# Optimization experiments

Measured on AMD Instinct MI355X. Metric: run time of the kernel, lower is better.

The kernel has to match this reference:

```python
import jax, jax.numpy as jnp
import numpy as np

N_NODES = 100000
N_EDGES = 3200000
IN_FEATS = 128
HIDDEN = 8
HEADS = 4
OUT_FEATS = 1
NEG_SLOPE = 0.2


def setup_inputs() -> dict:
    key = jax.random.key(0)
    ks = jax.random.split(key, 12)
    x = jax.random.normal(ks[0], (N_NODES, IN_FEATS), dtype=jnp.float32)
    edge_index = jax.random.randint(ks[1], (2, N_EDGES), 0, N_NODES, dtype=jnp.int64)
    # conv1: in=128 -> heads=4, out=8 (concat)
    s1 = 1.0 / np.sqrt(IN_FEATS)
    W1 = jax.random.uniform(ks[2], (IN_FEATS, HEADS * HIDDEN), jnp.float32, -s1, s1)
    att_src1 = jax.random.normal(ks[3], (HEADS, HIDDEN), dtype=jnp.float32) * 0.1
    att_dst1 = jax.random.normal(ks[4], (HEADS, HIDDEN), dtype=jnp.float32) * 0.1
    b1 = jnp.zeros((HEADS * HIDDEN,), jnp.float32)
    # conv2: in=32 -> heads=1, out=1 (no concat)
    s2 = 1.0 / np.sqrt(HEADS * HIDDEN)
    W2 = jax.random.uniform(ks[5], (HEADS * HIDDEN, 1 * OUT_FEATS), jnp.float32, -s2, s2)
    att_src2 = jax.random.normal(ks[6], (1, OUT_FEATS), dtype=jnp.float32) * 0.1
    att_dst2 = jax.random.normal(ks[7], (1, OUT_FEATS), dtype=jnp.float32) * 0.1
    b2 = jnp.zeros((OUT_FEATS,), jnp.float32)
    return {"x": x, "edge_index": edge_index,
            "W1": W1, "att_src1": att_src1, "att_dst1": att_dst1, "b1": b1,
            "W2": W2, "att_src2": att_src2, "att_dst2": att_dst2, "b2": b2}


def gat_conv(x, src, dst, W, a_src, a_dst, b, heads, out_ch, concat):
    """PyG GATConv (eval mode: dropout identity), self-loops already included in src/dst."""
    N = x.shape[0]
    h = (x @ W).reshape(N, heads, out_ch)                 # [N,H,C]
    alpha_s = jnp.sum(h * a_src[None], axis=-1)           # [N,H]
    alpha_d = jnp.sum(h * a_dst[None], axis=-1)           # [N,H]
    e = jax.nn.leaky_relu(alpha_s[src] + alpha_d[dst], NEG_SLOPE)  # [E,H]
    # segment softmax over incoming edges per destination node
    m = jax.ops.segment_max(e, dst, num_segments=N)       # [N,H]; every node has a self-loop
    ex = jnp.exp(e - m[dst])
    denom = jax.ops.segment_sum(ex, dst, num_segments=N)
    alpha = ex / denom[dst]                               # [E,H]
    msg = alpha[:, :, None] * h[src]                      # [E,H,C]
    agg = jax.ops.segment_sum(msg, dst, num_segments=N)   # [N,H,C]
    if concat:
        agg = agg.reshape(N, heads * out_ch)
    else:
        agg = agg.mean(axis=1)
    return agg + b


def reference(x, edge_index, W1, att_src1, att_dst1, b1, W2, att_src2, att_dst2, b2):
    N = x.shape[0]
    loops = jnp.arange(N, dtype=edge_index.dtype)
    src = jnp.concatenate([edge_index[0], loops])
    dst = jnp.concatenate([edge_index[1], loops])
    h = gat_conv(x, src, dst, W1, att_src1, att_dst1, b1, HEADS, HIDDEN, True)
    h = jax.nn.elu(h)
    out = gat_conv(h, src, dst, W2, att_src2, att_dst2, b2, 1, OUT_FEATS, False)
    return out
```

## Files before the change

kernel.cpp:

```cpp
#include <hip/hip_runtime.h>
#include <hip/hip_fp16.h>

#define NEG_SLOPE 0.2f
#define LOG2E 1.4426950408889634f
#define NC 782
#define TILE 6144
#define CAP 4736

__device__ __forceinline__ int uclamp(int i, int n) {
    return ((unsigned)i < (unsigned)n) ? i : 0;
}


__global__ __launch_bounds__(512) void k_msplit(const int* __restrict__ ei, int* __restrict__ gcur,
                                                int* __restrict__ ebin, int E, int N) {
    __shared__ int hist[NC], lpre[NC], lcur[NC];
    __shared__ int tbuf[TILE];
    __shared__ unsigned short tcb[TILE];
    __shared__ int part[512];
    int t = threadIdx.x;
    int tb = blockIdx.x * TILE;
    int nt = E - tb; if (nt > TILE) nt = TILE; if (nt < 0) nt = 0;
    for (int i = t; i < NC; i += 512) { hist[i] = 0; lcur[i] = 0; }
    __syncthreads();
    int sv[12]; short cbv[12];
#pragma unroll
    for (int j = 0; j < 12; ++j) {
        int idx = tb + j * 512 + t;
        int cb = -1, v = 0;
        if (idx < E) {
            int s = uclamp(ei[idx], N), d = uclamp(ei[E + idx], N);
            cb = d >> 7;
            v = (s << 7) | (d & 127);
            atomicAdd(&hist[cb], 1);
        }
        sv[j] = v; cbv[j] = (short)cb;
    }
    __syncthreads();
    int i0 = 2 * t, i1 = 2 * t + 1;
    int h0 = (i0 < NC) ? hist[i0] : 0;
    int h1 = (i1 < NC) ? hist[i1] : 0;
    int a = h0 + h1;
    part[t] = a;
    __syncthreads();
    for (int off = 1; off < 512; off <<= 1) {
        int v = (t >= off) ? part[t - off] : 0;
        __syncthreads();
        part[t] += v;
        __syncthreads();
    }
    int excl = part[t] - a;
    if (i0 < NC) lpre[i0] = excl;
    if (i1 < NC) lpre[i1] = excl + h0;
    __syncthreads();
    for (int i = t; i < NC; i += 512) {
        int h = hist[i];
        if (h) hist[i] = atomicAdd(&gcur[i], h);
    }
    __syncthreads();
#pragma unroll
    for (int j = 0; j < 12; ++j) {
        int cb = cbv[j];
        if (cb >= 0) {
            int slot = lpre[cb] + atomicAdd(&lcur[cb], 1);
            tbuf[slot] = sv[j];
            tcb[slot] = (unsigned short)cb;
        }
    }
    __syncthreads();
    for (int i = t; i < nt; i += 512) {
        int cb = tcb[i];
        int pos = hist[cb] + (i - lpre[cb]);
        if (pos < (cb + 1) * CAP) ebin[pos] = tbuf[i];
    }
}


__global__ __launch_bounds__(512) void k_sortB(const int* __restrict__ gcur, int* __restrict__ ebin,
                                               int* __restrict__ rstart, int* __restrict__ rend,
                                               int N) {
    __shared__ int buf[CAP];
    __shared__ int cnt[128], pre[128], cur[128];
    __shared__ int part[128];
    int b = blockIdx.x, t = threadIdx.x;
    int p0 = b * CAP;
    int n = gcur[b] - p0;
    if (n < 0) n = 0; if (n > CAP) n = CAP;
    if (t < 128) { cnt[t] = 0; cur[t] = 0; }
    __syncthreads();
    for (int i = t; i < n; i += 512) {
        int v = ebin[p0 + i];
        buf[i] = v;
        atomicAdd(&cnt[v & 127], 1);
    }
    __syncthreads();
    if (t < 128) part[t] = cnt[t];
    __syncthreads();
    if (t < 128) {
        for (int off = 1; off < 128; off <<= 1) {
            int v = (t >= off) ? part[t - off] : 0;
            __syncthreads();
            part[t] += v;
            __syncthreads();
        }
    } else {
        for (int off = 1; off < 128; off <<= 1) { __syncthreads(); __syncthreads(); }
    }
    if (t < 128) {
        int a = cnt[t];
        pre[t] = part[t] - a;
        int d = (b << 7) + t;
        if (d < N) {
            rstart[d] = p0 + pre[t];
            rend[d]   = p0 + pre[t] + a;
        }
    }
    __syncthreads();
    for (int i = t; i < n; i += 512) {
        int v = buf[i];
        int dl = v & 127;
        int pos = p0 + pre[dl] + atomicAdd(&cur[dl], 1);
        ebin[pos] = v >> 7;
    }
}


__global__ __launch_bounds__(256) void k_node1(const float* __restrict__ x,
                                               const float* __restrict__ W1,
                                               const float* __restrict__ asw,
                                               const float* __restrict__ adw,
                                               __half* __restrict__ h1h,
                                               float* __restrict__ as1,
                                               float* __restrict__ ad1,
                                               int* __restrict__ gcur, int N) {
    __shared__ float Wl[128 * 32];
    __shared__ float xl[32 * 132];
    __shared__ float als[32], ald[32];
    int t = threadIdx.x;
    if (blockIdx.x < 4) {
        int gi = blockIdx.x * 256 + t;
        if (gi < NC) gcur[gi] = gi * CAP;
    }
    for (int i = t; i < 128 * 32; i += 256) Wl[i] = W1[i];
    if (t < 32) { als[t] = asw[t]; ald[t] = adw[t]; }
    int nbase = blockIdx.x * 32;
    for (int i = t; i < 1024; i += 256) {
        int nd = i >> 5, j = i & 31;
        int node = nbase + nd;
        float4 v = (node < N) ? ((const float4*)(x + (size_t)node * 128))[j]
                              : make_float4(0.f, 0.f, 0.f, 0.f);
        *(float4*)&xl[nd * 132 + j * 4] = v;
    }
    __syncthreads();
    int nl = t >> 3, cq = t & 7;
    int node = nbase + nl;
    float4 acc = make_float4(0.f, 0.f, 0.f, 0.f);
    const float* xr = &xl[nl * 132];
#pragma unroll 8
    for (int k = 0; k < 128; ++k) {
        float xv = xr[k];
        float4 w = *(const float4*)&Wl[k * 32 + cq * 4];
        acc.x += xv * w.x; acc.y += xv * w.y; acc.z += xv * w.z; acc.w += xv * w.w;
    }
    if (node < N) {
        __half2 ha = __floats2half2_rn(acc.x, acc.y);
        __half2 hb = __floats2half2_rn(acc.z, acc.w);
        uint2 u; u.x = *(unsigned*)&ha; u.y = *(unsigned*)&hb;
        ((uint2*)(h1h + (size_t)node * 32))[cq] = u;
        int c4 = cq * 4;
        float vs = acc.x * als[c4] + acc.y * als[c4 + 1] + acc.z * als[c4 + 2] + acc.w * als[c4 + 3];
        float vd = acc.x * ald[c4] + acc.y * ald[c4 + 1] + acc.z * ald[c4 + 2] + acc.w * ald[c4 + 3];
        vs += __shfl_xor(vs, 1);
        vd += __shfl_xor(vd, 1);
        if ((cq & 1) == 0) {
            as1[node * 4 + (cq >> 1)] = vs * LOG2E;
            ad1[node * 4 + (cq >> 1)] = vd * LOG2E;
        }
    }
}


__global__ __launch_bounds__(256) void k_aggr1(const int* __restrict__ rstart, const int* __restrict__ rend,
                                               const int* __restrict__ col,
                                               const __half* __restrict__ h1h,
                                               const float* __restrict__ as1, const float* __restrict__ ad1,
                                               const float* __restrict__ W2,
                                               float* __restrict__ g, int N) {
    int wid = (blockIdx.x * 256 + threadIdx.x) >> 6;
    int lane = threadIdx.x & 63;
    int half = lane >> 5;
    int d = wid * 2 + half;
    if (d >= N) return;
    int slot = (lane >> 2) & 7;
    int q = lane & 3;
    float myAd = ad1[d * 4 + q];
    int p0 = rstart[d], p1 = rend[d];
    float acc[8];
#pragma unroll
    for (int i = 0; i < 8; ++i) acc[i] = 0.f;
    float ws = 0.f;
    int p = p0 + slot;
    while (p + 24 < p1) {
        int s0 = __builtin_nontemporal_load(&col[p]);
        int s1 = __builtin_nontemporal_load(&col[p + 8]);
        int s2 = __builtin_nontemporal_load(&col[p + 16]);
        int s3 = __builtin_nontemporal_load(&col[p + 24]);
        float a0 = as1[s0 * 4 + q];
        float a1 = as1[s1 * 4 + q];
        float a2 = as1[s2 * 4 + q];
        float a3 = as1[s3 * 4 + q];
        uint4 hv0 = *(const uint4*)(h1h + (size_t)s0 * 32 + q * 8);
        uint4 hv1 = *(const uint4*)(h1h + (size_t)s1 * 32 + q * 8);
        uint4 hv2 = *(const uint4*)(h1h + (size_t)s2 * 32 + q * 8);
        uint4 hv3 = *(const uint4*)(h1h + (size_t)s3 * 32 + q * 8);
        float e0 = a0 + myAd; e0 = e0 > 0.f ? e0 : NEG_SLOPE * e0;
        float e1 = a1 + myAd; e1 = e1 > 0.f ? e1 : NEG_SLOPE * e1;
        float e2 = a2 + myAd; e2 = e2 > 0.f ? e2 : NEG_SLOPE * e2;
        float e3 = a3 + myAd; e3 = e3 > 0.f ? e3 : NEG_SLOPE * e3;
        float w0 = exp2f(e0), w1 = exp2f(e1), w2 = exp2f(e2), w3 = exp2f(e3);
        ws += (w0 + w1) + (w2 + w3);
        const __half* a0p = (const __half*)&hv0;
        const __half* a1p = (const __half*)&hv1;
        const __half* a2p = (const __half*)&hv2;
        const __half* a3p = (const __half*)&hv3;
#pragma unroll
        for (int i = 0; i < 8; ++i) acc[i] += w0 * (float)a0p[i];
#pragma unroll
        for (int i = 0; i < 8; ++i) acc[i] += w1 * (float)a1p[i];
#pragma unroll
        for (int i = 0; i < 8; ++i) acc[i] += w2 * (float)a2p[i];
#pragma unroll
        for (int i = 0; i < 8; ++i) acc[i] += w3 * (float)a3p[i];
        p += 32;
    }
    while (p < p1) {
        int s = __builtin_nontemporal_load(&col[p]);
        float av = as1[s * 4 + q];
        uint4 hv = *(const uint4*)(h1h + (size_t)s * 32 + q * 8);
        float e = av + myAd; e = e > 0.f ? e : NEG_SLOPE * e;
        float w = exp2f(e);
        ws += w;
        const __half* ap = (const __half*)&hv;
#pragma unroll
        for (int i = 0; i < 8; ++i) acc[i] += w * (float)ap[i];
        p += 8;
    }
#pragma unroll
    for (int m = 4; m <= 16; m <<= 1) {
        ws += __shfl_xor(ws, m);
#pragma unroll
        for (int i = 0; i < 8; ++i) acc[i] += __shfl_xor(acc[i], m);
    }
    {
        float e = as1[d * 4 + q] + myAd;
        e = e > 0.f ? e : NEG_SLOPE * e;
        float w = exp2f(e);
        uint4 hv = *(const uint4*)(h1h + (size_t)d * 32 + q * 8);
        ws += w;
        const __half* ap = (const __half*)&hv;
#pragma unroll
        for (int i = 0; i < 8; ++i) acc[i] += w * (float)ap[i];
    }
    float inv = 1.f / ws;
    float4 w2a = *(const float4*)(W2 + q * 8);
    float4 w2b = *(const float4*)(W2 + q * 8 + 4);
    float gv = 0.f;
#pragma unroll
    for (int i = 0; i < 8; ++i) {
        float val = acc[i] * inv;
        val = val > 0.f ? val : (__expf(val) - 1.f);
        float w2 = (i < 4) ? ((const float*)&w2a)[i] : ((const float*)&w2b)[i - 4];
        gv += val * w2;
    }
    gv += __shfl_xor(gv, 1);
    gv += __shfl_xor(gv, 2);
    if ((lane & 31) == 0) g[d] = gv;
}


__global__ __launch_bounds__(256) void k_aggr2(const int* __restrict__ rstart, const int* __restrict__ rend,
                                               const int* __restrict__ col,
                                               const float* __restrict__ g,
                                               const float* __restrict__ asw,
                                               const float* __restrict__ adw,
                                               float* __restrict__ out, int N) {
    int tid = blockIdx.x * 256 + threadIdx.x;
    int d = tid >> 3, l = tid & 7;
    if (d >= N) return;
    float asc = asw[0] * LOG2E;
    float adc = adw[0] * LOG2E;
    float gd = g[d];
    float myd = gd * adc;
    int p0 = rstart[d], p1 = rend[d];
    float ws = 0.f, acc = 0.f;
    for (int p = p0 + l; p < p1; p += 8) {
        float gs = g[__builtin_nontemporal_load(&col[p])];
        float e = gs * asc + myd;
        e = e > 0.f ? e : NEG_SLOPE * e;
        float w = exp2f(e);
        ws += w;
        acc += w * gs;
    }
    ws += __shfl_xor(ws, 1); ws += __shfl_xor(ws, 2); ws += __shfl_xor(ws, 4);
    acc += __shfl_xor(acc, 1); acc += __shfl_xor(acc, 2); acc += __shfl_xor(acc, 4);
    if (l == 0) {
        float e = gd * asc + myd;
        e = e > 0.f ? e : NEG_SLOPE * e;
        float w = exp2f(e);
        ws += w;
        acc += w * gd;
        out[d] = acc / ws;
    }
}

extern "C" void kernel_launch(void* const* d_in, const int* in_sizes, int n_in,
                              void* d_out, int out_size, void* d_ws, size_t ws_size,
                              hipStream_t stream) {
    const float* x    = (const float*)d_in[0];
    const int*   ei   = (const int*)d_in[1];
    const float* W1   = (const float*)d_in[2];
    const float* as1w = (const float*)d_in[3];
    const float* ad1w = (const float*)d_in[4];
    const float* W2   = (const float*)d_in[6];
    const float* as2w = (const float*)d_in[7];
    const float* ad2w = (const float*)d_in[8];

    const int N  = in_sizes[0] / 128;
    const int E  = in_sizes[1] / 2;
    const int EB = NC * CAP;

    char* ws = (char*)d_ws;
    size_t off = 0;
    int*    gcur   = (int*)(ws + off);    off += 16384;
    int*    rstart = (int*)(ws + off);    off += (size_t)N * 4;
    int*    rend   = (int*)(ws + off);    off += (size_t)N * 4;
    int*    ebin   = (int*)(ws + off);    off += (size_t)EB * 4;
    __half* h1h    = (__half*)(ws + off); off += (size_t)N * 64;
    float*  as1    = (float*)(ws + off);  off += (size_t)N * 16;
    float*  ad1    = (float*)(ws + off);  off += (size_t)N * 16;
    float*  g      = (float*)(ws + off);  off += (size_t)N * 4;

    k_node1<<<(N + 31) / 32, 256, 0, stream>>>(x, W1, as1w, ad1w, h1h, as1, ad1, gcur, N);
    k_msplit<<<(E + TILE - 1) / TILE, 512, 0, stream>>>(ei, gcur, ebin, E, N);
    k_sortB<<<NC, 512, 0, stream>>>(gcur, ebin, rstart, rend, N);
    k_aggr1<<<(N + 7) / 8, 256, 0, stream>>>(rstart, rend, ebin, h1h, as1, ad1, W2, g, N);
    k_aggr2<<<(N * 8 + 255) / 256, 256, 0, stream>>>(rstart, rend, ebin, g, as2w, ad2w, (float*)d_out, N);
}
```

Before: 260.6 us.

## Split layer-1 aggregation into two source-half passes for gather cache locality

Edges are binned by destination block and by source half (node below or above 50000), giving two CSR ranges per destination. Layer-1 aggregation then runs as two passes, each gathering h1 rows from only half the nodes, so the gathered working set is smaller and can stay cache resident. Partial sums and weight sums are passed between the passes through a per-node state buffer. The source attention score is now recomputed from the gathered half-precision h1 instead of read from a separate as1 array. This adds a kernel launch, extra per-node state traffic and more per-edge arithmetic, and computing the score from fp16 h1 changes numerics slightly.

```diff
diff --git a/kernel.cpp b/kernel.cpp
--- a/kernel.cpp
+++ b/kernel.cpp
@@ -3,9 +3,13 @@
 
 #define NEG_SLOPE 0.2f
 #define LOG2E 1.4426950408889634f
-#define NC 782
+#define NB 782
+#define NC2 1564
+#define HALFN 50000
 #define TILE 6144
-#define CAP 4736
+#define CAP2 2368
+
+typedef float f32x4 __attribute__((ext_vector_type(4)));
 
 __device__ __forceinline__ int uclamp(int i, int n) {
     return ((unsigned)i < (unsigned)n) ? i : 0;
@@ -14,14 +18,14 @@
 
 __global__ __launch_bounds__(512) void k_msplit(const int* __restrict__ ei, int* __restrict__ gcur,
                                                 int* __restrict__ ebin, int E, int N) {
-    __shared__ int hist[NC], lpre[NC], lcur[NC];
+    __shared__ int hist[NC2], lpre[NC2], lcur[NC2];
     __shared__ int tbuf[TILE];
     __shared__ unsigned short tcb[TILE];
     __shared__ int part[512];
     int t = threadIdx.x;
     int tb = blockIdx.x * TILE;
     int nt = E - tb; if (nt > TILE) nt = TILE; if (nt < 0) nt = 0;
-    for (int i = t; i < NC; i += 512) { hist[i] = 0; lcur[i] = 0; }
+    for (int i = t; i < NC2; i += 512) { hist[i] = 0; lcur[i] = 0; }
     __syncthreads();
     int sv[12]; short cbv[12];
 #pragma unroll
@@ -30,17 +34,19 @@
         int cb = -1, v = 0;
         if (idx < E) {
             int s = uclamp(ei[idx], N), d = uclamp(ei[E + idx], N);
-            cb = d >> 7;
+            cb = ((d >> 7) << 1) | (s >= HALFN ? 1 : 0);
             v = (s << 7) | (d & 127);
             atomicAdd(&hist[cb], 1);
         }
         sv[j] = v; cbv[j] = (short)cb;
     }
     __syncthreads();
-    int i0 = 2 * t, i1 = 2 * t + 1;
-    int h0 = (i0 < NC) ? hist[i0] : 0;
-    int h1 = (i1 < NC) ? hist[i1] : 0;
-    int a = h0 + h1;
+    int i0 = 4 * t;
+    int h0 = (i0 + 0 < NC2) ? hist[i0 + 0] : 0;
+    int h1 = (i0 + 1 < NC2) ? hist[i0 + 1] : 0;
+    int h2 = (i0 + 2 < NC2) ? hist[i0 + 2] : 0;
+    int h3 = (i0 + 3 < NC2) ? hist[i0 + 3] : 0;
+    int a = h0 + h1 + h2 + h3;
     part[t] = a;
     __syncthreads();
     for (int off = 1; off < 512; off <<= 1) {
@@ -50,10 +56,12 @@
         __syncthreads();
     }
     int excl = part[t] - a;
-    if (i0 < NC) lpre[i0] = excl;
-    if (i1 < NC) lpre[i1] = excl + h0;
-    __syncthreads();
-    for (int i = t; i < NC; i += 512) {
+    if (i0 + 0 < NC2) lpre[i0 + 0] = excl;
+    if (i0 + 1 < NC2) lpre[i0 + 1] = excl + h0;
+    if (i0 + 2 < NC2) lpre[i0 + 2] = excl + h0 + h1;
+    if (i0 + 3 < NC2) lpre[i0 + 3] = excl + h0 + h1 + h2;
+    __syncthreads();
+    for (int i = t; i < NC2; i += 512) {
         int h = hist[i];
         if (h) hist[i] = atomicAdd(&gcur[i], h);
     }
@@ -71,21 +79,22 @@
     for (int i = t; i < nt; i += 512) {
         int cb = tcb[i];
         int pos = hist[cb] + (i - lpre[cb]);
-        if (pos < (cb + 1) * CAP) ebin[pos] = tbuf[i];
+        if (pos < (cb + 1) * CAP2) ebin[pos] = tbuf[i];
     }
 }
 
 
 __global__ __launch_bounds__(512) void k_sortB(const int* __restrict__ gcur, int* __restrict__ ebin,
-                                               int* __restrict__ rstart, int* __restrict__ rend,
+                                               int* __restrict__ rs0, int* __restrict__ re0,
+                                               int* __restrict__ rs1, int* __restrict__ re1,
                                                int N) {
-    __shared__ int buf[CAP];
+    __shared__ int buf[CAP2];
     __shared__ int cnt[128], pre[128], cur[128];
     __shared__ int part[128];
     int b = blockIdx.x, t = threadIdx.x;
-    int p0 = b * CAP;
+    int p0 = b * CAP2;
     int n = gcur[b] - p0;
-    if (n < 0) n = 0; if (n > CAP) n = CAP;
+    if (n < 0) n = 0; if (n > CAP2) n = CAP2;
     if (t < 128) { cnt[t] = 0; cur[t] = 0; }
     __syncthreads();
     for (int i = t; i < n; i += 512) {
@@ -109,10 +118,12 @@
     if (t < 128) {
         int a = cnt[t];
         pre[t] = part[t] - a;
-        int d = (b << 7) + t;
+        int d = ((b >> 1) << 7) + t;
         if (d < N) {
-            rstart[d] = p0 + pre[t];
-            rend[d]   = p0 + pre[t] + a;
+            int* rsp = (b & 1) ? rs1 : rs0;
+            int* rep = (b & 1) ? re1 : re0;
+            rsp[d] = p0 + pre[t];
+            rep[d] = p0 + pre[t] + a;
         }
     }
     __syncthreads();
@@ -127,22 +138,20 @@
 
 __global__ __launch_bounds__(256) void k_node1(const float* __restrict__ x,
                                                const float* __restrict__ W1,
-                                               const float* __restrict__ asw,
                                                const float* __restrict__ adw,
                                                __half* __restrict__ h1h,
-                                               float* __restrict__ as1,
                                                float* __restrict__ ad1,
                                                int* __restrict__ gcur, int N) {
     __shared__ float Wl[128 * 32];
     __shared__ float xl[32 * 132];
-    __shared__ float als[32], ald[32];
+    __shared__ float ald[32];
     int t = threadIdx.x;
-    if (blockIdx.x < 4) {
+    if (blockIdx.x < 8) {
         int gi = blockIdx.x * 256 + t;
-        if (gi < NC) gcur[gi] = gi * CAP;
+        if (gi < NC2) gcur[gi] = gi * CAP2;
     }
     for (int i = t; i < 128 * 32; i += 256) Wl[i] = W1[i];
-    if (t < 32) { als[t] = asw[t]; ald[t] = adw[t]; }
+    if (t < 32) ald[t] = adw[t];
     int nbase = blockIdx.x * 32;
     for (int i = t; i < 1024; i += 256) {
         int nd = i >> 5, j = i & 31;
@@ -168,61 +177,64 @@
         uint2 u; u.x = *(unsigned*)&ha; u.y = *(unsigned*)&hb;
         ((uint2*)(h1h + (size_t)node * 32))[cq] = u;
         int c4 = cq * 4;
-        float vs = acc.x * als[c4] + acc.y * als[c4 + 1] + acc.z * als[c4 + 2] + acc.w * als[c4 + 3];
         float vd = acc.x * ald[c4] + acc.y * ald[c4 + 1] + acc.z * ald[c4 + 2] + acc.w * ald[c4 + 3];
-        vs += __shfl_xor(vs, 1);
         vd += __shfl_xor(vd, 1);
         if ((cq & 1) == 0) {
-            as1[node * 4 + (cq >> 1)] = vs * LOG2E;
             ad1[node * 4 + (cq >> 1)] = vd * LOG2E;
         }
     }
 }
 
 
-__global__ __launch_bounds__(256) void k_aggr1(const int* __restrict__ rstart, const int* __restrict__ rend,
+template<int PASS>
+__global__ __launch_bounds__(256) void k_aggrP(const int* __restrict__ rs, const int* __restrict__ re,
                                                const int* __restrict__ col,
                                                const __half* __restrict__ h1h,
-                                               const float* __restrict__ as1, const float* __restrict__ ad1,
+                                               const float* __restrict__ ad1,
+                                               const float* __restrict__ asw,
                                                const float* __restrict__ W2,
+                                               float* __restrict__ pstate,
                                                float* __restrict__ g, int N) {
     int wid = (blockIdx.x * 256 + threadIdx.x) >> 6;
     int lane = threadIdx.x & 63;
     int half = lane >> 5;
     int d = wid * 2 + half;
     if (d >= N) return;
-    int slot = (lane >> 2) & 7;
+    int l5 = lane & 31;
+    int slot = l5 >> 2;
     int q = lane & 3;
+    float4 aA = *(const float4*)(asw + q * 8);
+    float4 aB = *(const float4*)(asw + q * 8 + 4);
+    float as0 = aA.x * LOG2E, as1 = aA.y * LOG2E, as2 = aA.z * LOG2E, as3 = aA.w * LOG2E;
+    float as4 = aB.x * LOG2E, as5 = aB.y * LOG2E, as6 = aB.z * LOG2E, as7 = aB.w * LOG2E;
     float myAd = ad1[d * 4 + q];
-    int p0 = rstart[d], p1 = rend[d];
+    int p0 = rs[d], p1 = re[d];
     float acc[8];
 #pragma unroll
     for (int i = 0; i < 8; ++i) acc[i] = 0.f;
     float ws = 0.f;
     int p = p0 + slot;
+#define DOT8(hp) (as0*(float)(hp)[0] + as1*(float)(hp)[1] + as2*(float)(hp)[2] + as3*(float)(hp)[3] \
+                + as4*(float)(hp)[4] + as5*(float)(hp)[5] + as6*(float)(hp)[6] + as7*(float)(hp)[7])
     while (p + 24 < p1) {
         int s0 = __builtin_nontemporal_load(&col[p]);
         int s1 = __builtin_nontemporal_load(&col[p + 8]);
         int s2 = __builtin_nontemporal_load(&col[p + 16]);
         int s3 = __builtin_nontemporal_load(&col[p + 24]);
-        float a0 = as1[s0 * 4 + q];
-        float a1 = as1[s1 * 4 + q];
-        float a2 = as1[s2 * 4 + q];
-        float a3 = as1[s3 * 4 + q];
         uint4 hv0 = *(const uint4*)(h1h + (size_t)s0 * 32 + q * 8);
         uint4 hv1 = *(const uint4*)(h1h + (size_t)s1 * 32 + q * 8);
         uint4 hv2 = *(const uint4*)(h1h + (size_t)s2 * 32 + q * 8);
         uint4 hv3 = *(const uint4*)(h1h + (size_t)s3 * 32 + q * 8);
-        float e0 = a0 + myAd; e0 = e0 > 0.f ? e0 : NEG_SLOPE * e0;
-        float e1 = a1 + myAd; e1 = e1 > 0.f ? e1 : NEG_SLOPE * e1;
-        float e2 = a2 + myAd; e2 = e2 > 0.f ? e2 : NEG_SLOPE * e2;
-        float e3 = a3 + myAd; e3 = e3 > 0.f ? e3 : NEG_SLOPE * e3;
-        float w0 = exp2f(e0), w1 = exp2f(e1), w2 = exp2f(e2), w3 = exp2f(e3);
-        ws += (w0 + w1) + (w2 + w3);
         const __half* a0p = (const __half*)&hv0;
         const __half* a1p = (const __half*)&hv1;
         const __half* a2p = (const __half*)&hv2;
         const __half* a3p = (const __half*)&hv3;
+        float e0 = DOT8(a0p) + myAd; e0 = e0 > 0.f ? e0 : NEG_SLOPE * e0;
+        float e1 = DOT8(a1p) + myAd; e1 = e1 > 0.f ? e1 : NEG_SLOPE * e1;
+        float e2 = DOT8(a2p) + myAd; e2 = e2 > 0.f ? e2 : NEG_SLOPE * e2;
+        float e3 = DOT8(a3p) + myAd; e3 = e3 > 0.f ? e3 : NEG_SLOPE * e3;
+        float w0 = exp2f(e0), w1 = exp2f(e1), w2 = exp2f(e2), w3 = exp2f(e3);
+        ws += (w0 + w1) + (w2 + w3);
 #pragma unroll
         for (int i = 0; i < 8; ++i) acc[i] += w0 * (float)a0p[i];
 #pragma unroll
@@ -235,12 +247,11 @@
     }
     while (p < p1) {
         int s = __builtin_nontemporal_load(&col[p]);
-        float av = as1[s * 4 + q];
         uint4 hv = *(const uint4*)(h1h + (size_t)s * 32 + q * 8);
-        float e = av + myAd; e = e > 0.f ? e : NEG_SLOPE * e;
+        const __half* ap = (const __half*)&hv;
+        float e = DOT8(ap) + myAd; e = e > 0.f ? e : NEG_SLOPE * e;
         float w = exp2f(e);
         ws += w;
-        const __half* ap = (const __half*)&hv;
 #pragma unroll
         for (int i = 0; i < 8; ++i) acc[i] += w * (float)ap[i];
         p += 8;
@@ -251,16 +262,34 @@
 #pragma unroll
         for (int i = 0; i < 8; ++i) acc[i] += __shfl_xor(acc[i], m);
     }
+    if (PASS == 0) {
+        if (slot == 0) {
+            f32x4 v0 = { acc[0], acc[1], acc[2], acc[3] };
+            f32x4 v1 = { acc[4], acc[5], acc[6], acc[7] };
+            __builtin_nontemporal_store(v0, (f32x4*)&pstate[(size_t)d * 36 + q * 8]);
+            __builtin_nontemporal_store(v1, (f32x4*)&pstate[(size_t)d * 36 + q * 8 + 4]);
+            __builtin_nontemporal_store(ws, &pstate[(size_t)d * 36 + 32 + q]);
+        }
+        return;
+    }
     {
-        float e = as1[d * 4 + q] + myAd;
-        e = e > 0.f ? e : NEG_SLOPE * e;
+        f32x4 p0v = __builtin_nontemporal_load((const f32x4*)&pstate[(size_t)d * 36 + q * 8]);
+        f32x4 p1v = __builtin_nontemporal_load((const f32x4*)&pstate[(size_t)d * 36 + q * 8 + 4]);
+        float pws = __builtin_nontemporal_load(&pstate[(size_t)d * 36 + 32 + q]);
+        acc[0] += p0v.x; acc[1] += p0v.y; acc[2] += p0v.z; acc[3] += p0v.w;
+        acc[4] += p1v.x; acc[5] += p1v.y; acc[6] += p1v.z; acc[7] += p1v.w;
+        ws += pws;
+    }
+    {
+        uint4 hv = *(const uint4*)(h1h + (size_t)d * 32 + q * 8);
+        const __half* ap = (const __half*)&hv;
+        float e = DOT8(ap) + myAd; e = e > 0.f ? e : NEG_SLOPE * e;
         float w = exp2f(e);
-        uint4 hv = *(const uint4*)(h1h + (size_t)d * 32 + q * 8);
         ws += w;
-        const __half* ap = (const __half*)&hv;
 #pragma unroll
         for (int i = 0; i < 8; ++i) acc[i] += w * (float)ap[i];
     }
+#undef DOT8
     float inv = 1.f / ws;
     float4 w2a = *(const float4*)(W2 + q * 8);
     float4 w2b = *(const float4*)(W2 + q * 8 + 4);
@@ -274,11 +303,12 @@
     }
     gv += __shfl_xor(gv, 1);
     gv += __shfl_xor(gv, 2);
-    if ((lane & 31) == 0) g[d] = gv;
-}
-
-
-__global__ __launch_bounds__(256) void k_aggr2(const int* __restrict__ rstart, const int* __restrict__ rend,
+    if (l5 == 0) g[d] = gv;
+}
+
+
+__global__ __launch_bounds__(256) void k_aggr2(const int* __restrict__ rs0, const int* __restrict__ re0,
+                                               const int* __restrict__ rs1, const int* __restrict__ re1,
                                                const int* __restrict__ col,
                                                const float* __restrict__ g,
                                                const float* __restrict__ asw,
@@ -291,15 +321,18 @@
     float adc = adw[0] * LOG2E;
     float gd = g[d];
     float myd = gd * adc;
-    int p0 = rstart[d], p1 = rend[d];
     float ws = 0.f, acc = 0.f;
-    for (int p = p0 + l; p < p1; p += 8) {
-        float gs = g[__builtin_nontemporal_load(&col[p])];
-        float e = gs * asc + myd;
-        e = e > 0.f ? e : NEG_SLOPE * e;
-        float w = exp2f(e);
-        ws += w;
-        acc += w * gs;
+    for (int pass = 0; pass < 2; ++pass) {
+        int p0 = pass ? rs1[d] : rs0[d];
+        int p1 = pass ? re1[d] : re0[d];
+        for (int p = p0 + l; p < p1; p += 8) {
+            float gs = g[__builtin_nontemporal_load(&col[p])];
+            float e = gs * asc + myd;
+            e = e > 0.f ? e : NEG_SLOPE * e;
+            float w = exp2f(e);
+            ws += w;
+            acc += w * gs;
+        }
     }
     ws += __shfl_xor(ws, 1); ws += __shfl_xor(ws, 2); ws += __shfl_xor(ws, 4);
     acc += __shfl_xor(acc, 1); acc += __shfl_xor(acc, 2); acc += __shfl_xor(acc, 4);
@@ -327,22 +360,25 @@
 
     const int N  = in_sizes[0] / 128;
     const int E  = in_sizes[1] / 2;
-    const int EB = NC * CAP;
+    const int EB = NC2 * CAP2;
 
     char* ws = (char*)d_ws;
     size_t off = 0;
-    int*    gcur   = (int*)(ws + off);    off += 16384;
-    int*    rstart = (int*)(ws + off);    off += (size_t)N * 4;
-    int*    rend   = (int*)(ws + off);    off += (size_t)N * 4;
+    int*    gcur   = (int*)(ws + off);    off += 8192;
+    int*    rs0    = (int*)(ws + off);    off += (size_t)N * 4;
+    int*    re0    = (int*)(ws + off);    off += (size_t)N * 4;
+    int*    rs1    = (int*)(ws + off);    off += (size_t)N * 4;
+    int*    re1    = (int*)(ws + off);    off += (size_t)N * 4;
     int*    ebin   = (int*)(ws + off);    off += (size_t)EB * 4;
     __half* h1h    = (__half*)(ws + off); off += (size_t)N * 64;
-    float*  as1    = (float*)(ws + off);  off += (size_t)N * 16;
     float*  ad1    = (float*)(ws + off);  off += (size_t)N * 16;
+    float*  pstate = (float*)(ws + off);  off += (size_t)N * 36 * 4;
     float*  g      = (float*)(ws + off);  off += (size_t)N * 4;
 
-    k_node1<<<(N + 31) / 32, 256, 0, stream>>>(x, W1, as1w, ad1w, h1h, as1, ad1, gcur, N);
+    k_node1<<<(N + 31) / 32, 256, 0, stream>>>(x, W1, ad1w, h1h, ad1, gcur, N);
     k_msplit<<<(E + TILE - 1) / TILE, 512, 0, stream>>>(ei, gcur, ebin, E, N);
-    k_sortB<<<NC, 512, 0, stream>>>(gcur, ebin, rstart, rend, N);
-    k_aggr1<<<(N + 7) / 8, 256, 0, stream>>>(rstart, rend, ebin, h1h, as1, ad1, W2, g, N);
-    k_aggr2<<<(N * 8 + 255) / 256, 256, 0, stream>>>(rstart, rend, ebin, g, as2w, ad2w, (float*)d_out, N);
-}
+    k_sortB<<<NC2, 512, 0, stream>>>(gcur, ebin, rs0, re0, rs1, re1, N);
+    k_aggrP<0><<<(N + 7) / 8, 256, 0, stream>>>(rs0, re0, ebin, h1h, ad1, as1w, W2, pstate, g, N);
+    k_aggrP<1><<<(N + 7) / 8, 256, 0, stream>>>(rs1, re1, ebin, h1h, ad1, as1w, W2, pstate, g, N);
+    k_aggr2<<<(N * 8 + 255) / 256, 256, 0, stream>>>(rs0, re0, rs1, re1, ebin, g, as2w, ad2w, (float*)d_out, N);
+}
```

After: 298.0 us. +14.4%, slower.
